# Kernel tuning notes

Hardware: AMD Instinct MI355X
Metric: run time of the kernel (lower is better)

The kernel has to match this reference:

```python
import jax, jax.numpy as jnp
import numpy as np

N = 50000        # nodes
E = 1600000      # edges (before self loops)
IN_DIM = 300     # input feature size
HID = 256        # hidden size
HEADS = 8
OC = HID // HEADS  # out channels per head = 32
LAYERS = 4
B = 1024         # number of target pairs
C = 3            # num classes
NEG_SLOPE = 0.2  # PyG GATConv leaky_relu slope


def setup_inputs() -> dict:
    key = jax.random.key(0)
    ks = jax.random.split(key, 12)

    def glorot(k, shape):
        lim = np.sqrt(6.0 / (shape[-2] + shape[-1]))
        return jax.random.uniform(k, shape, jnp.float32, -lim, lim)

    return {
        "x": jax.random.normal(ks[0], (N, IN_DIM), jnp.float32),
        "edge_index": jax.random.randint(ks[1], (2, E), 0, N, jnp.int64 if jax.config.jax_enable_x64 else jnp.int32),
        "target_mask": jax.random.randint(ks[2], (B, 2), 0, N, jnp.int64 if jax.config.jax_enable_x64 else jnp.int32),
        # lin1: [IN_DIM, HID] (stored pre-transposed vs torch)
        "lin1_W": glorot(ks[3], (IN_DIM, HID)),
        "lin1_b": jnp.zeros((HID,), jnp.float32),
        # stacked GATConv params
        "convs_W": glorot(ks[4], (LAYERS, HID, HEADS * OC)),
        "convs_att_dst": glorot(ks[5], (LAYERS, HEADS, OC)),  # att half applied to x_i (target)
        "convs_att_src": glorot(ks[6], (LAYERS, HEADS, OC)),  # att half applied to x_j (source)
        "convs_b": jnp.zeros((LAYERS, HID), jnp.float32),
        # lin3: [2*HID, C]
        "lin3_W": glorot(ks[7], (2 * HID, C)),
        "lin3_b": jnp.zeros((C,), jnp.float32),
    }


def gat_layer(h, src, tgt, W, att_dst, att_src, bias):
    """PyG-style GATConv (concat heads), edge list already includes self loops.
    h: [N, HID]; src/tgt: [E+N]; W: [HID, HEADS*OC]."""
    hw = (h @ W).reshape(N, HEADS, OC)
    # per-node attention scores, gathered per-edge (avoids materializing concat features)
    s_dst = jnp.einsum("nho,ho->nh", hw, att_dst)  # score for target role
    s_src = jnp.einsum("nho,ho->nh", hw, att_src)  # score for source role
    alpha = jax.nn.leaky_relu(s_dst[tgt] + s_src[src], NEG_SLOPE)  # [Etot, HEADS]
    # softmax over edges sharing the same target node (self loops => no empty segments)
    m = jax.ops.segment_max(alpha, tgt, num_segments=N)
    ex = jnp.exp(alpha - m[tgt])
    denom = jax.ops.segment_sum(ex, tgt, num_segments=N)
    a = ex / (denom[tgt] + 1e-16)
    # weighted scatter-aggregate of source features
    out = jax.ops.segment_sum(hw[src] * a[:, :, None], tgt, num_segments=N)  # [N, HEADS, OC]
    return out.reshape(N, HEADS * OC) + bias


def reference(x, edge_index, target_mask, lin1_W, lin1_b, convs_W,
              convs_att_dst, convs_att_src, convs_b, lin3_W, lin3_b):
    # add self loops once (PyG GATConv does this per layer; same edge set every layer)
    loop = jnp.arange(N, dtype=edge_index.dtype)
    src = jnp.concatenate([edge_index[0], loop])
    tgt = jnp.concatenate([edge_index[1], loop])

    h = x @ lin1_W + lin1_b
    for l in range(LAYERS):
        h = jax.nn.elu(gat_layer(h, src, tgt, convs_W[l],
                                 convs_att_dst[l], convs_att_src[l], convs_b[l]))
    # gather the two target nodes per sample and flatten -> [B, 2*HID]
    feats = h[target_mask].reshape(B, 2 * HID)
    logits = feats @ lin3_W + lin3_b
    return logits
```

## Files before the change

### kernel.cpp

```cpp
#include <hip/hip_runtime.h>
#include <math.h>

#define N_NODES 50000
#define N_PAD   50048
#define E_EDGES 1600000
#define ETOT    (E_EDGES + N_NODES)
#define EPAD    (E_EDGES + 8 * N_NODES)
#define IN_DIM  300
#define KP1     320
#define HID     256
#define HEADS   8
#define OC      32
#define LAYERS  4
#define BSAMP   1024
#define NEG_SLOPE 0.2f
#define NS1     (N_NODES + 1)

#define NB     8
#define NPB    6250
#define BCAP   262144
#define NBLK_P 512
#define NBLK_S 196
#define NBLK_B 2048
#define NAGG   2048

typedef unsigned long long ull;
typedef unsigned short u16;
typedef _Float16 half8 __attribute__((ext_vector_type(8)));
typedef _Float16 half4v __attribute__((ext_vector_type(4)));
typedef float f32x4 __attribute__((ext_vector_type(4)));

#define GLDS16(g, l) __builtin_amdgcn_global_load_lds( \
    (const __attribute__((address_space(1))) void*)(g), \
    (__attribute__((address_space(3))) void*)(l), 16, 0, 0)


__global__ __launch_bounds__(256) void part_count_kernel(const int* __restrict__ tgt,
                                                         int* __restrict__ gcount) {
    __shared__ int cnt[NB];
    if (threadIdx.x < NB) cnt[threadIdx.x] = 0;
    __syncthreads();
    const int chunk = (ETOT + NBLK_P - 1) / NBLK_P;
    int beg = blockIdx.x * chunk;
    int end = min(beg + chunk, ETOT);
    for (int e = beg + threadIdx.x; e < end; e += 256) {
        int t_ = (e < E_EDGES) ? tgt[e] : (e - E_EDGES);
        atomicAdd(&cnt[t_ / NPB], 1);
    }
    __syncthreads();
    if (threadIdx.x < NB) gcount[blockIdx.x * NB + threadIdx.x] = cnt[threadIdx.x];
}

__global__ __launch_bounds__(512) void part_scan_kernel(const int* __restrict__ gcount,
                                                        int* __restrict__ goff,
                                                        int* __restrict__ bcnt) {
    __shared__ int arr[NBLK_P][NB];
    int k = threadIdx.x;
    int4 a = ((const int4*)gcount)[k * 2];
    int4 b = ((const int4*)gcount)[k * 2 + 1];
    int own[NB] = {a.x, a.y, a.z, a.w, b.x, b.y, b.z, b.w};
    #pragma unroll
    for (int j = 0; j < NB; j++) arr[k][j] = own[j];
    __syncthreads();
    for (int off = 1; off < NBLK_P; off <<= 1) {
        int tmp[NB];
        #pragma unroll
        for (int j = 0; j < NB; j++) tmp[j] = (k >= off) ? arr[k - off][j] : 0;
        __syncthreads();
        #pragma unroll
        for (int j = 0; j < NB; j++) arr[k][j] += tmp[j];
        __syncthreads();
    }
    int ex[NB];
    #pragma unroll
    for (int j = 0; j < NB; j++) ex[j] = arr[k][j] - own[j];
    ((int4*)goff)[k * 2]     = make_int4(ex[0], ex[1], ex[2], ex[3]);
    ((int4*)goff)[k * 2 + 1] = make_int4(ex[4], ex[5], ex[6], ex[7]);
    if (k == NBLK_P - 1) {
        #pragma unroll
        for (int j = 0; j < NB; j++) bcnt[j] = arr[k][j];
    }
}

__global__ __launch_bounds__(256) void part_scatter_kernel(const int* __restrict__ src,
                                                           const int* __restrict__ tgt,
                                                           const int* __restrict__ goff,
                                                           ull* __restrict__ bpart) {
    __shared__ int cur[NB];
    if (threadIdx.x < NB) cur[threadIdx.x] = goff[blockIdx.x * NB + threadIdx.x];
    __syncthreads();
    const int chunk = (ETOT + NBLK_P - 1) / NBLK_P;
    int beg = blockIdx.x * chunk;
    int end = min(beg + chunk, ETOT);
    for (int e = beg + threadIdx.x; e < end; e += 256) {
        int s_, t_;
        if (e < E_EDGES) { s_ = src[e]; t_ = tgt[e]; }
        else             { s_ = t_ = e - E_EDGES; }
        int b = t_ / NPB;
        int pos = atomicAdd(&cur[b], 1);
        bpart[(size_t)b * BCAP + pos] = ((ull)(unsigned)t_ << 32) | (unsigned)s_;
    }
}

__global__ __launch_bounds__(256) void count_edges_kernel(const ull* __restrict__ bpart,
                                                          const int* __restrict__ bcnt,
                                                          int* counts) {
    int b = blockIdx.x & (NB - 1);
    int ib = blockIdx.x >> 3;
    int nblk = gridDim.x >> 3;
    int nb = bcnt[b];
    const ull* bp = bpart + (size_t)b * BCAP;
    for (int i = ib * 256 + threadIdx.x; i < nb; i += nblk * 256)
        atomicAdd(&counts[(int)(bp[i] >> 32)], 1);
}

__global__ __launch_bounds__(256) void scan1_kernel(const int* __restrict__ counts,
                                                    int* __restrict__ row_ptr,
                                                    int* __restrict__ bsum) {
    __shared__ int sums[256];
    int t = threadIdx.x;
    int i = blockIdx.x * 256 + t;
    int c = (i < N_NODES) ? ((counts[i] + 7) & ~7) : 0;
    sums[t] = c;
    __syncthreads();
    for (int off = 1; off < 256; off <<= 1) {
        int a = sums[t];
        int u = (t >= off) ? sums[t - off] : 0;
        __syncthreads();
        sums[t] = a + u;
        __syncthreads();
    }
    if (i < N_NODES) row_ptr[i] = sums[t] - c;
    if (t == 255) bsum[blockIdx.x] = sums[255];
}

__global__ __launch_bounds__(256) void scan2_kernel(const int* __restrict__ bsum,
                                                    int* __restrict__ boff,
                                                    int* __restrict__ row_ptr) {
    __shared__ int sums[256];
    int t = threadIdx.x;
    int b = (t < NBLK_S) ? bsum[t] : 0;
    sums[t] = b;
    __syncthreads();
    for (int off = 1; off < 256; off <<= 1) {
        int a = sums[t];
        int u = (t >= off) ? sums[t - off] : 0;
        __syncthreads();
        sums[t] = a + u;
        __syncthreads();
    }
    if (t < NBLK_S) boff[t] = sums[t] - b;
    if (t == 255) row_ptr[N_NODES] = sums[255];
}

__global__ __launch_bounds__(256) void scan3_kernel(int* __restrict__ row_ptr,
                                                    const int* __restrict__ boff,
                                                    int* __restrict__ cursor) {
    int i = blockIdx.x * 256 + threadIdx.x;
    if (i >= N_NODES) return;
    int v = row_ptr[i] + boff[blockIdx.x];
    row_ptr[i] = v;
    cursor[i]  = v;
}

__global__ __launch_bounds__(256) void fill_edges_kernel(const ull* __restrict__ bpart,
                                                         const int* __restrict__ bcnt,
                                                         int* cursor, u16* __restrict__ col) {
    int b = blockIdx.x & (NB - 1);
    int ib = blockIdx.x >> 3;
    int nblk = gridDim.x >> 3;
    int nb = bcnt[b];
    const ull* bp = bpart + (size_t)b * BCAP;
    for (int i = ib * 256 + threadIdx.x; i < nb; i += nblk * 256) {
        ull pk = bp[i];
        int t_ = (int)(pk >> 32);
        int s_ = (int)pk;
        int pos = atomicAdd(&cursor[t_], 1);
        col[pos] = (u16)s_;
    }
}

__global__ __launch_bounds__(256) void pad_edges_kernel(const int* __restrict__ cursor,
                                                        const int* __restrict__ row_ptr,
                                                        u16* __restrict__ col) {
    int i = blockIdx.x * 256 + threadIdx.x;
    if (i >= N_NODES) return;
    int e = cursor[i];
    int pe = row_ptr[i + 1];
    for (; e < pe; e++) col[e] = (u16)N_NODES;
}


__global__ __launch_bounds__(256) void cast_x_kernel(const float* __restrict__ x, _Float16* __restrict__ xh) {
    int i = blockIdx.x * 256 + threadIdx.x;
    if (i >= N_NODES * (KP1 / 8)) return;
    int r = i / (KP1 / 8), c8 = i % (KP1 / 8);
    half8 o;
    const float4* xr = (const float4*)(x + (size_t)r * IN_DIM);
    if (c8 < 37) {
        float4 u = xr[c8 * 2], v = xr[c8 * 2 + 1];
        o[0] = (_Float16)u.x; o[1] = (_Float16)u.y; o[2] = (_Float16)u.z; o[3] = (_Float16)u.w;
        o[4] = (_Float16)v.x; o[5] = (_Float16)v.y; o[6] = (_Float16)v.z; o[7] = (_Float16)v.w;
    } else if (c8 == 37) {
        float4 u = xr[74];
        o[0] = (_Float16)u.x; o[1] = (_Float16)u.y; o[2] = (_Float16)u.z; o[3] = (_Float16)u.w;
        o[4] = o[5] = o[6] = o[7] = (_Float16)0.f;
    } else {
        #pragma unroll
        for (int j = 0; j < 8; j++) o[j] = (_Float16)0.f;
    }
    ((half8*)xh)[i] = o;
}

__global__ __launch_bounds__(256) void cast_w1_kernel(const float* __restrict__ W, _Float16* __restrict__ Wt) {
    int i = blockIdx.x * 256 + threadIdx.x;
    if (i >= HID * KP1) return;
    int n = i / KP1, k = i % KP1;
    float v = (k < IN_DIM) ? W[(size_t)k * HID + n] : 0.f;
    Wt[i] = (_Float16)v;
}

__global__ __launch_bounds__(256) void cast_wc_kernel(const float* __restrict__ W, _Float16* __restrict__ Wt) {
    int i = blockIdx.x * 256 + threadIdx.x;
    if (i >= LAYERS * HID * HID) return;
    int l = i / (HID * HID);
    int r = i % (HID * HID);
    int n = r / HID, k = r % HID;
    Wt[i] = (_Float16)W[(size_t)l * HID * HID + (size_t)k * HID + n];
}

__global__ __launch_bounds__(256) void gemm_mfma_kernel(const _Float16* __restrict__ A,
                                                        const _Float16* __restrict__ Wt,
                                                        const float* __restrict__ bias,
                                                        _Float16* __restrict__ C,
                                                        int M, int Kp, int addbias,
                                                        int headmajor) {
    __shared__ _Float16 As[128][32];
    __shared__ _Float16 Bs[128][32];
    const int tid = threadIdx.x;
    const int m0 = blockIdx.x * 128;
    const int n0 = blockIdx.y * 128;
    const int w = tid >> 6, lane = tid & 63;
    const int wm = (w & 1) * 64, wn = (w >> 1) * 64;
    const int quad = lane >> 4, m16 = lane & 15;

    f32x4 acc[4][4];
    #pragma unroll
    for (int i = 0; i < 4; i++)
        #pragma unroll
        for (int j = 0; j < 4; j++)
            acc[i][j] = (f32x4){0.f, 0.f, 0.f, 0.f};

    char* lA = (char*)&As[0][0] + w * 1024;
    char* lB = (char*)&Bs[0][0] + w * 1024;

    for (int k0 = 0; k0 < Kp; k0 += 32) {
        #pragma unroll
        for (int i = 0; i < 2; i++) {
            int seg = tid + i * 256;
            int row = seg >> 2, off = seg & 3;
            GLDS16(&A[(size_t)(m0 + row) * Kp + k0 + off * 8], lA + i * 4096);
            GLDS16(&Wt[(size_t)(n0 + row) * Kp + k0 + off * 8], lB + i * 4096);
        }
        __syncthreads();

        half8 af[4], bf[4];
        #pragma unroll
        for (int i = 0; i < 4; i++) {
            af[i] = *(const half8*)&As[wm + i * 16 + m16][quad * 8];
            bf[i] = *(const half8*)&Bs[wn + i * 16 + m16][quad * 8];
        }
        #pragma unroll
        for (int mi = 0; mi < 4; mi++)
            #pragma unroll
            for (int ni = 0; ni < 4; ni++)
                acc[mi][ni] = __builtin_amdgcn_mfma_f32_16x16x32_f16(af[mi], bf[ni], acc[mi][ni], 0, 0, 0);
        __syncthreads();
    }

    #pragma unroll
    for (int mi = 0; mi < 4; mi++) {
        #pragma unroll
        for (int r = 0; r < 4; r++) {
            int row = m0 + wm + mi * 16 + quad * 4 + r;
            if (row < M) {
                #pragma unroll
                for (int ni = 0; ni < 4; ni++) {
                    int colg = n0 + wn + ni * 16 + m16;
                    float v = acc[mi][ni][r];
                    if (addbias) v += bias[colg];
                    if (headmajor) {
                        int hd = colg >> 5, oc = colg & 31;
                        C[((size_t)hd * N_NODES + row) * 32 + oc] = (_Float16)v;
                    } else {
                        C[(size_t)row * HID + colg] = (_Float16)v;
                    }
                }
            }
        }
    }
}

__global__ __launch_bounds__(256) void score_kernel(const _Float16* __restrict__ hw,
                                                    const float* __restrict__ att_dst,
                                                    const float* __restrict__ att_src,
                                                    float* __restrict__ s_dst,
                                                    float* __restrict__ s_src) {
    if (blockIdx.x == 0 && threadIdx.x < HEADS)
        s_src[(size_t)threadIdx.x * NS1 + N_NODES] = -1e30f;
    int wv = threadIdx.x >> 6, lane = threadIdx.x & 63;
    int nd = lane >> 3, hd = lane & 7;
    float4 ad[8], as4[8];
    const float4* A4d = (const float4*)att_dst;
    const float4* A4s = (const float4*)att_src;
    #pragma unroll
    for (int j = 0; j < 8; j++) { ad[j] = A4d[hd * 8 + j]; as4[j] = A4s[hd * 8 + j]; }
    const half8* hw8 = (const half8*)hw;
    int nwaves = gridDim.x * 4;
    for (int g = blockIdx.x * 4 + wv; g < N_NODES / 8; g += nwaves) {
        int node = g * 8 + nd;
        float sd = 0.f, ss = 0.f;
        #pragma unroll
        for (int k = 0; k < 4; k++) {
            half8 v = hw8[((size_t)hd * N_NODES + node) * 4 + k];
            #pragma unroll
            for (int i = 0; i < 8; i++) {
                float f = (float)v[i];
                int q = k * 8 + i;
                sd += f * ((const float*)&ad[q >> 2])[q & 3];
                ss += f * ((const float*)&as4[q >> 2])[q & 3];
            }
        }
        s_dst[(size_t)hd * N_NODES + node] = sd;
        s_src[(size_t)hd * NS1 + node] = ss;
    }
}

__global__ __launch_bounds__(256, 8) void agg_kernel(const int* __restrict__ row_ptr,
                                                     const u16* __restrict__ col,
                                                     const float* __restrict__ s_dst,
                                                     const float* __restrict__ s_src,
                                                     const _Float16* __restrict__ hw,
                                                     const float* __restrict__ bias,
                                                     _Float16* __restrict__ h_out) {
    __shared__ float exL[4][2][128];
    __shared__ int   snL[4][2][128];

    const int wv   = threadIdx.x >> 6;
    const int lane = threadIdx.x & 63;
    const int head = blockIdx.x & (NB - 1);
    const int ib   = blockIdx.x >> 3;
    const int nh   = lane >> 5;
    const int es   = (lane >> 2) & 7;
    const int cl   = lane & 3;
    const int wid  = ib * 4 + wv;
    const int NW   = (NAGG / NB) * 4;

    const float* sdh = s_dst + (size_t)head * N_NODES;
    const float* ssh = s_src + (size_t)head * NS1;
    const char*  hwh = (const char*)(hw + (size_t)head * N_NODES * 32);
    const unsigned vcl = (unsigned)(cl * 16);

    float bb[8];
    {
        const float* bpt = bias + head * 32 + cl * 8;
        #pragma unroll
        for (int i = 0; i < 8; i++) bb[i] = bpt[i];
    }

    float* exw = &exL[wv][nh][0];
    int*   snw = &snL[wv][nh][0];

    auto stage = [&](int s, int startg, int csz, float sdv) {
        float* exd = &exL[wv][s][0];
        int*   snd = &snL[wv][s][0];
        for (int b = 0; b < csz; b += 64) {
            int slot = b + lane;
            if (slot < csz) {
                int sn = (int)col[startg + slot];
                float a = sdv + ssh[(unsigned)sn];
                a = fmaxf(a, NEG_SLOPE * a);
                exd[slot] = __expf(a);
                snd[slot] = sn << 6;
            }
        }
    };

    float dsum, a0, a1, a2, a3, a4, a5, a6, a7;

    auto phaseC = [&](int ngrp) {
        int d0 = snw[es];
        int d1 = (ngrp > 1) ? snw[8 + es] : 0;
        half8 v0 = *(const half8*)(hwh + ((unsigned)d0 | vcl));
        for (int g = 0; g < ngrp; g++) {
            int d2 = (g + 2 < ngrp) ? snw[(g + 2) * 8 + es] : 0;
            half8 vn = *(const half8*)(hwh + ((unsigned)d1 | vcl));
            float e = exw[g * 8 + es];
            dsum += e;
            a0 += e * (float)v0[0];
            a1 += e * (float)v0[1];
            a2 += e * (float)v0[2];
            a3 += e * (float)v0[3];
            a4 += e * (float)v0[4];
            a5 += e * (float)v0[5];
            a6 += e * (float)v0[6];
            a7 += e * (float)v0[7];
            v0 = vn; d1 = d2;
        }
    };

    for (int tb = wid * 2; tb < N_NODES; tb += NW * 2) {
        int r0 = row_ptr[tb];
        int r1 = row_ptr[tb + 1];
        int r2 = row_ptr[tb + 2];
        int pd0 = r1 - r0, pd1 = r2 - r1;
        float sdv0 = sdh[tb], sdv1 = sdh[tb + 1];

        dsum = 0.f;
        a0 = a1 = a2 = a3 = a4 = a5 = a6 = a7 = 0.f;

        if (pd0 <= 128 && pd1 <= 128) {
            int mx = max(pd0, pd1);
            stage(0, r0, pd0, sdv0);
            stage(1, r1, pd1, sdv1);
            for (int slot = pd0 + lane; slot < mx; slot += 64) {
                exL[wv][0][slot] = 0.f; snL[wv][0][slot] = 0;
            }
            for (int slot = pd1 + lane; slot < mx; slot += 64) {
                exL[wv][1][slot] = 0.f; snL[wv][1][slot] = 0;
            }
            phaseC(mx >> 3);
        } else {
            #pragma unroll 1
            for (int s = 0; s < 2; s++) {
                for (int slot = lane; slot < 128; slot += 64) {
                    exL[wv][s ^ 1][slot] = 0.f; snL[wv][s ^ 1][slot] = 0;
                }
                int rs = s ? r1 : r0;
                int pds = s ? pd1 : pd0;
                float sdvs = s ? sdv1 : sdv0;
                for (int c0 = 0; c0 < pds; c0 += 128) {
                    int csz = min(pds - c0, 128);
                    stage(s, rs + c0, csz, sdvs);
                    phaseC(csz >> 3);
                }
            }
        }

        #pragma unroll
        for (int off = 4; off <= 16; off <<= 1) {
            dsum += __shfl_xor(dsum, off);
            a0 += __shfl_xor(a0, off);
            a1 += __shfl_xor(a1, off);
            a2 += __shfl_xor(a2, off);
            a3 += __shfl_xor(a3, off);
            a4 += __shfl_xor(a4, off);
            a5 += __shfl_xor(a5, off);
            a6 += __shfl_xor(a6, off);
            a7 += __shfl_xor(a7, off);
        }

        if (es == 0) {
            float inv = 1.f / (dsum + 1e-16f);
            float o[8] = {a0 * inv + bb[0], a1 * inv + bb[1],
                          a2 * inv + bb[2], a3 * inv + bb[3],
                          a4 * inv + bb[4], a5 * inv + bb[5],
                          a6 * inv + bb[6], a7 * inv + bb[7]};
            half8 ov;
            #pragma unroll
            for (int i = 0; i < 8; i++) {
                float v = (o[i] > 0.f) ? o[i] : (__expf(o[i]) - 1.f);
                ov[i] = (_Float16)v;
            }
            *(half8*)(h_out + (size_t)(tb + nh) * HID + head * 32 + cl * 8) = ov;
        }
    }
}

__global__ __launch_bounds__(256) void head_kernel(const _Float16* __restrict__ h,
                                                   const int* __restrict__ target_mask,
                                                   const float* __restrict__ W,
                                                   const float* __restrict__ b,
                                                   float* __restrict__ out) {
    int s = blockIdx.x;
    int t = threadIdx.x;
    int n0 = target_mask[s * 2 + 0];
    int n1 = target_mask[s * 2 + 1];
    float f0 = (float)h[(size_t)n0 * HID + t];
    float f1 = (float)h[(size_t)n1 * HID + t];
    float a0 = f0 * W[t * 3 + 0] + f1 * W[(t + 256) * 3 + 0];
    float a1 = f0 * W[t * 3 + 1] + f1 * W[(t + 256) * 3 + 1];
    float a2 = f0 * W[t * 3 + 2] + f1 * W[(t + 256) * 3 + 2];
    #pragma unroll
    for (int off = 32; off >= 1; off >>= 1) {
        a0 += __shfl_xor(a0, off);
        a1 += __shfl_xor(a1, off);
        a2 += __shfl_xor(a2, off);
    }
    __shared__ float red[4][3];
    int wv = t >> 6, ln = t & 63;
    if (ln == 0) { red[wv][0] = a0; red[wv][1] = a1; red[wv][2] = a2; }
    __syncthreads();
    if (t < 3) {
        out[s * 3 + t] = red[0][t] + red[1][t] + red[2][t] + red[3][t] + b[t];
    }
}


extern "C" void kernel_launch(void* const* d_in, const int* in_sizes, int n_in,
                              void* d_out, int out_size, void* d_ws, size_t ws_size,
                              hipStream_t stream) {
    const float* x        = (const float*)d_in[0];
    const int*   eidx     = (const int*)  d_in[1];
    const int*   tmask    = (const int*)  d_in[2];
    const float* lin1_W   = (const float*)d_in[3];
    const float* lin1_b   = (const float*)d_in[4];
    const float* convs_W  = (const float*)d_in[5];
    const float* att_dst  = (const float*)d_in[6];
    const float* att_src  = (const float*)d_in[7];
    const float* convs_b  = (const float*)d_in[8];
    const float* lin3_W   = (const float*)d_in[9];
    const float* lin3_b   = (const float*)d_in[10];
    float* out = (float*)d_out;

    char* ws = (char*)d_ws;
    size_t off = 0;
    auto alloc = [&](size_t bytes) -> void* {
        void* p = ws + off;
        off = (off + bytes + 255) & ~(size_t)255;
        return p;
    };
    _Float16* xh   = (_Float16*)alloc((size_t)N_PAD * KP1 * 2);
    _Float16* h    = (_Float16*)alloc((size_t)N_PAD * HID * 2);
    _Float16* hw   = (_Float16*)alloc((size_t)N_PAD * HID * 2);
    _Float16* w1t  = (_Float16*)alloc((size_t)HID * KP1 * 2);
    _Float16* wct  = (_Float16*)alloc((size_t)LAYERS * HID * HID * 2);
    float* sdst    = (float*)alloc((size_t)HEADS * N_NODES * 4);
    float* ssrc    = (float*)alloc((size_t)HEADS * NS1 * 4);
    int*   counts  = (int*)  alloc((size_t)N_NODES * 4);
    int*   rowptr  = (int*)  alloc((size_t)(N_NODES + 1) * 4);
    int*   cursor  = (int*)  alloc((size_t)N_NODES * 4);
    u16*   col     = (u16*)  alloc((size_t)(EPAD + 32) * 2);
    ull*   bpart   = (ull*)  alloc((size_t)NB * BCAP * 8);
    int*   bcnt    = (int*)  alloc((size_t)NB * 4);
    int*   gcount  = (int*)  alloc((size_t)NBLK_P * NB * 4);
    int*   goff    = (int*)  alloc((size_t)NBLK_P * NB * 4);
    int*   bsum    = (int*)  alloc((size_t)NBLK_S * 4);
    int*   boff    = (int*)  alloc((size_t)NBLK_S * 4);

    const int* src = eidx;
    const int* tgt = eidx + E_EDGES;

    hipMemsetAsync(counts, 0, (size_t)N_NODES * 4, stream);
    part_count_kernel<<<NBLK_P, 256, 0, stream>>>(tgt, gcount);
    part_scan_kernel<<<1, NBLK_P, 0, stream>>>(gcount, goff, bcnt);
    part_scatter_kernel<<<NBLK_P, 256, 0, stream>>>(src, tgt, goff, bpart);
    count_edges_kernel<<<NBLK_B, 256, 0, stream>>>(bpart, bcnt, counts);
    scan1_kernel<<<NBLK_S, 256, 0, stream>>>(counts, rowptr, bsum);
    scan2_kernel<<<1, 256, 0, stream>>>(bsum, boff, rowptr);
    scan3_kernel<<<NBLK_S, 256, 0, stream>>>(rowptr, boff, cursor);
    fill_edges_kernel<<<NBLK_B, 256, 0, stream>>>(bpart, bcnt, cursor, col);
    pad_edges_kernel<<<(N_NODES + 255) / 256, 256, 0, stream>>>(cursor, rowptr, col);

    cast_x_kernel<<<(N_NODES * (KP1 / 8) + 255) / 256, 256, 0, stream>>>(x, xh);
    cast_w1_kernel<<<(HID * KP1 + 255) / 256, 256, 0, stream>>>(lin1_W, w1t);
    cast_wc_kernel<<<(LAYERS * HID * HID + 255) / 256, 256, 0, stream>>>(convs_W, wct);

    gemm_mfma_kernel<<<dim3((N_NODES + 127) / 128, HID / 128), 256, 0, stream>>>(
        xh, w1t, lin1_b, h, N_NODES, KP1, 1, 0);

    for (int l = 0; l < LAYERS; l++) {
        gemm_mfma_kernel<<<dim3((N_NODES + 127) / 128, HID / 128), 256, 0, stream>>>(
            h, wct + (size_t)l * HID * HID, nullptr, hw, N_NODES, HID, 0, 1);
        score_kernel<<<512, 256, 0, stream>>>(
            hw, att_dst + (size_t)l * HEADS * OC, att_src + (size_t)l * HEADS * OC, sdst, ssrc);
        agg_kernel<<<NAGG, 256, 0, stream>>>(
            rowptr, col, sdst, ssrc, hw, convs_b + (size_t)l * HID, h);
    }

    head_kernel<<<BSAMP, 256, 0, stream>>>(h, tmask, lin3_W, lin3_b, out);
}
```

Before: 988.9 us.

## Software-pipeline GAT aggregation: prefetch next node pair's edges into double-buffered LDS

```diff
diff --git a/kernel.cpp b/kernel.cpp
--- a/kernel.cpp
+++ b/kernel.cpp
@@ -22,12 +22,12 @@
 #define NBLK_P 512
 #define NBLK_S 196
 #define NBLK_B 2048
-#define NAGG   2048
+#define NAGG   1536
+#define NW2    ((NAGG / NB) * 4 * 2)
 
 typedef unsigned long long ull;
 typedef unsigned short u16;
 typedef _Float16 half8 __attribute__((ext_vector_type(8)));
-typedef _Float16 half4v __attribute__((ext_vector_type(4)));
 typedef float f32x4 __attribute__((ext_vector_type(4)));
 
 #define GLDS16(g, l) __builtin_amdgcn_global_load_lds( \
@@ -336,15 +336,14 @@
     }
 }
 
-__global__ __launch_bounds__(256, 8) void agg_kernel(const int* __restrict__ row_ptr,
+__global__ __launch_bounds__(256, 6) void agg_kernel(const int* __restrict__ row_ptr,
                                                      const u16* __restrict__ col,
                                                      const float* __restrict__ s_dst,
                                                      const float* __restrict__ s_src,
                                                      const _Float16* __restrict__ hw,
                                                      const float* __restrict__ bias,
                                                      _Float16* __restrict__ h_out) {
-    __shared__ float exL[4][2][128];
-    __shared__ int   snL[4][2][128];
+    __shared__ ull pkL[4][2][2][128];
 
     const int wv   = threadIdx.x >> 6;
     const int lane = threadIdx.x & 63;
@@ -354,48 +353,31 @@
     const int es   = (lane >> 2) & 7;
     const int cl   = lane & 3;
     const int wid  = ib * 4 + wv;
-    const int NW   = (NAGG / NB) * 4;
 
     const float* sdh = s_dst + (size_t)head * N_NODES;
     const float* ssh = s_src + (size_t)head * NS1;
     const char*  hwh = (const char*)(hw + (size_t)head * N_NODES * 32);
     const unsigned vcl = (unsigned)(cl * 16);
 
-    float bb[8];
-    {
-        const float* bpt = bias + head * 32 + cl * 8;
-        #pragma unroll
-        for (int i = 0; i < 8; i++) bb[i] = bpt[i];
-    }
-
-    float* exw = &exL[wv][nh][0];
-    int*   snw = &snL[wv][nh][0];
-
-    auto stage = [&](int s, int startg, int csz, float sdv) {
-        float* exd = &exL[wv][s][0];
-        int*   snd = &snL[wv][s][0];
-        for (int b = 0; b < csz; b += 64) {
-            int slot = b + lane;
-            if (slot < csz) {
-                int sn = (int)col[startg + slot];
-                float a = sdv + ssh[(unsigned)sn];
-                a = fmaxf(a, NEG_SLOPE * a);
-                exd[slot] = __expf(a);
-                snd[slot] = sn << 6;
-            }
+    float dsum, a0, a1, a2, a3, a4, a5, a6, a7;
+
+    auto wr = [&](ull* pkd, int slot, int mx_, float sdv, float ss, int sn) {
+        if (slot < mx_) {
+            float a = sdv + ss;
+            a = fmaxf(a, NEG_SLOPE * a);
+            float ex = __expf(a);
+            pkd[slot] = ((ull)__float_as_uint(ex) << 32) | (unsigned)(sn << 6);
         }
     };
 
-    float dsum, a0, a1, a2, a3, a4, a5, a6, a7;
-
-    auto phaseC = [&](int ngrp) {
-        int d0 = snw[es];
-        int d1 = (ngrp > 1) ? snw[8 + es] : 0;
-        half8 v0 = *(const half8*)(hwh + ((unsigned)d0 | vcl));
+    auto phaseC = [&](const ull* pkw, int ngrp) {
+        ull p0 = pkw[es];
+        ull p1 = (ngrp > 1) ? pkw[8 + es] : 0;
+        half8 v0 = *(const half8*)(hwh + ((unsigned)(p0 & 0xffffffffu) | vcl));
         for (int g = 0; g < ngrp; g++) {
-            int d2 = (g + 2 < ngrp) ? snw[(g + 2) * 8 + es] : 0;
-            half8 vn = *(const half8*)(hwh + ((unsigned)d1 | vcl));
-            float e = exw[g * 8 + es];
+            ull p2 = (g + 2 < ngrp) ? pkw[(g + 2) * 8 + es] : 0;
+            half8 vn = *(const half8*)(hwh + ((unsigned)(p1 & 0xffffffffu) | vcl));
+            float e = __uint_as_float((unsigned)(p0 >> 32));
             dsum += e;
             a0 += e * (float)v0[0];
             a1 += e * (float)v0[1];
@@ -405,48 +387,11 @@
             a5 += e * (float)v0[5];
             a6 += e * (float)v0[6];
             a7 += e * (float)v0[7];
-            v0 = vn; d1 = d2;
+            p0 = p1; p1 = p2; v0 = vn;
         }
     };
 
-    for (int tb = wid * 2; tb < N_NODES; tb += NW * 2) {
-        int r0 = row_ptr[tb];
-        int r1 = row_ptr[tb + 1];
-        int r2 = row_ptr[tb + 2];
-        int pd0 = r1 - r0, pd1 = r2 - r1;
-        float sdv0 = sdh[tb], sdv1 = sdh[tb + 1];
-
-        dsum = 0.f;
-        a0 = a1 = a2 = a3 = a4 = a5 = a6 = a7 = 0.f;
-
-        if (pd0 <= 128 && pd1 <= 128) {
-            int mx = max(pd0, pd1);
-            stage(0, r0, pd0, sdv0);
-            stage(1, r1, pd1, sdv1);
-            for (int slot = pd0 + lane; slot < mx; slot += 64) {
-                exL[wv][0][slot] = 0.f; snL[wv][0][slot] = 0;
-            }
-            for (int slot = pd1 + lane; slot < mx; slot += 64) {
-                exL[wv][1][slot] = 0.f; snL[wv][1][slot] = 0;
-            }
-            phaseC(mx >> 3);
-        } else {
-            #pragma unroll 1
-            for (int s = 0; s < 2; s++) {
-                for (int slot = lane; slot < 128; slot += 64) {
-                    exL[wv][s ^ 1][slot] = 0.f; snL[wv][s ^ 1][slot] = 0;
-                }
-                int rs = s ? r1 : r0;
-                int pds = s ? pd1 : pd0;
-                float sdvs = s ? sdv1 : sdv0;
-                for (int c0 = 0; c0 < pds; c0 += 128) {
-                    int csz = min(pds - c0, 128);
-                    stage(s, rs + c0, csz, sdvs);
-                    phaseC(csz >> 3);
-                }
-            }
-        }
-
+    auto finish = [&](int tbp) {
         #pragma unroll
         for (int off = 4; off <= 16; off <<= 1) {
             dsum += __shfl_xor(dsum, off);
@@ -459,22 +404,124 @@
             a6 += __shfl_xor(a6, off);
             a7 += __shfl_xor(a7, off);
         }
-
         if (es == 0) {
+            const float* bpt = bias + head * 32 + cl * 8;
             float inv = 1.f / (dsum + 1e-16f);
-            float o[8] = {a0 * inv + bb[0], a1 * inv + bb[1],
-                          a2 * inv + bb[2], a3 * inv + bb[3],
-                          a4 * inv + bb[4], a5 * inv + bb[5],
-                          a6 * inv + bb[6], a7 * inv + bb[7]};
+            float o[8] = {a0 * inv + bpt[0], a1 * inv + bpt[1],
+                          a2 * inv + bpt[2], a3 * inv + bpt[3],
+                          a4 * inv + bpt[4], a5 * inv + bpt[5],
+                          a6 * inv + bpt[6], a7 * inv + bpt[7]};
             half8 ov;
             #pragma unroll
             for (int i = 0; i < 8; i++) {
                 float v = (o[i] > 0.f) ? o[i] : (__expf(o[i]) - 1.f);
                 ov[i] = (_Float16)v;
             }
-            *(half8*)(h_out + (size_t)(tb + nh) * HID + head * 32 + cl * 8) = ov;
-        }
-    }
+            *(half8*)(h_out + (size_t)(tbp + nh) * HID + head * 32 + cl * 8) = ov;
+        }
+    };
+
+    int cbig, cmx, cr0, cr1, cpd0, cpd1;
+    float csd0, csd1;
+    int tb = wid * 2;
+
+    {
+        cr0 = row_ptr[tb]; cr1 = row_ptr[tb + 1];
+        int r2 = row_ptr[tb + 2];
+        cpd0 = cr1 - cr0; cpd1 = r2 - cr1;
+        csd0 = sdh[tb]; csd1 = sdh[tb + 1];
+        cbig = (cpd0 > 128) || (cpd1 > 128);
+        cmx = max(cpd0, cpd1);
+        if (!cbig) {
+            int sA = N_NODES, sB = N_NODES, sC = N_NODES, sD = N_NODES;
+            if (lane < cpd0)      sA = (int)col[cr0 + lane];
+            if (lane + 64 < cpd0) sB = (int)col[cr0 + lane + 64];
+            if (lane < cpd1)      sC = (int)col[cr1 + lane];
+            if (lane + 64 < cpd1) sD = (int)col[cr1 + lane + 64];
+            float eA = ssh[(unsigned)sA], eB = ssh[(unsigned)sB];
+            float eC = ssh[(unsigned)sC], eD = ssh[(unsigned)sD];
+            wr(&pkL[wv][0][0][0], lane,      cmx, csd0, eA, sA);
+            wr(&pkL[wv][0][0][0], lane + 64, cmx, csd0, eB, sB);
+            wr(&pkL[wv][0][1][0], lane,      cmx, csd1, eC, sC);
+            wr(&pkL[wv][0][1][0], lane + 64, cmx, csd1, eD, sD);
+        }
+    }
+
+#define AGG_PROC(CUR, NXT)                                                     \
+    do {                                                                       \
+        int tn = tb + NW2;                                                     \
+        bool hn = tn < N_NODES;                                                \
+        int nbig = 0, nmx = 0, nr0 = 0, nr1 = 0, npd0 = 0, npd1 = 0;           \
+        float nsd0 = 0.f, nsd1 = 0.f;                                          \
+        int sA = N_NODES, sB = N_NODES, sC = N_NODES, sD = N_NODES;            \
+        if (hn) {                                                              \
+            nr0 = row_ptr[tn]; nr1 = row_ptr[tn + 1];                          \
+            int r2n = row_ptr[tn + 2];                                         \
+            npd0 = nr1 - nr0; npd1 = r2n - nr1;                                \
+            nsd0 = sdh[tn]; nsd1 = sdh[tn + 1];                                \
+            nbig = (npd0 > 128) || (npd1 > 128);                               \
+            nmx = max(npd0, npd1);                                             \
+            if (!nbig) {                                                       \
+                if (lane < npd0)      sA = (int)col[nr0 + lane];               \
+                if (lane + 64 < npd0) sB = (int)col[nr0 + lane + 64];          \
+                if (lane < npd1)      sC = (int)col[nr1 + lane];               \
+                if (lane + 64 < npd1) sD = (int)col[nr1 + lane + 64];          \
+            }                                                                  \
+        }                                                                      \
+        float eA = ssh[(unsigned)sA], eB = ssh[(unsigned)sB];                  \
+        float eC = ssh[(unsigned)sC], eD = ssh[(unsigned)sD];                  \
+        dsum = 0.f;                                                            \
+        a0 = a1 = a2 = a3 = a4 = a5 = a6 = a7 = 0.f;                           \
+        if (!cbig) {                                                           \
+            phaseC(&pkL[wv][CUR][nh][0], cmx >> 3);                            \
+        } else {                                                               \
+            for (int slot = lane; slot < 128; slot += 64) {                    \
+                pkL[wv][CUR][0][slot] = 0ull;                                  \
+                pkL[wv][CUR][1][slot] = 0ull;                                  \
+            }                                                                  \
+            for (int s = 0; s < 2; s++) {                                      \
+                int rs = s ? cr1 : cr0;                                        \
+                int pds = s ? cpd1 : cpd0;                                     \
+                float sdvs = s ? csd1 : csd0;                                  \
+                for (int c0 = 0; c0 < pds; c0 += 128) {                        \
+                    int csz = min(pds - c0, 128);                              \
+                    for (int b = 0; b < csz; b += 64) {                        \
+                        int slot = b + lane;                                   \
+                        if (slot < csz) {                                      \
+                            int sn = (int)col[rs + c0 + slot];                 \
+                            float a = sdvs + ssh[(unsigned)sn];                \
+                            a = fmaxf(a, NEG_SLOPE * a);                       \
+                            pkL[wv][CUR][s][slot] =                            \
+                                ((ull)__float_as_uint(__expf(a)) << 32) |      \
+                                (unsigned)(sn << 6);                           \
+                        }                                                      \
+                    }                                                          \
+                    phaseC(&pkL[wv][CUR][nh][0], csz >> 3);                    \
+                }                                                              \
+                for (int slot = lane; slot < 128; slot += 64)                  \
+                    pkL[wv][CUR][s][slot] = 0ull;                              \
+            }                                                                  \
+        }                                                                      \
+        if (hn && !nbig) {                                                     \
+            wr(&pkL[wv][NXT][0][0], lane,      nmx, nsd0, eA, sA);             \
+            wr(&pkL[wv][NXT][0][0], lane + 64, nmx, nsd0, eB, sB);             \
+            wr(&pkL[wv][NXT][1][0], lane,      nmx, nsd1, eC, sC);             \
+            wr(&pkL[wv][NXT][1][0], lane + 64, nmx, nsd1, eD, sD);             \
+        }                                                                      \
+        finish(tb);                                                            \
+        cbig = nbig; cmx = nmx; cr0 = nr0; cr1 = nr1;                          \
+        cpd0 = npd0; cpd1 = npd1; csd0 = nsd0; csd1 = nsd1;                    \
+    } while (0)
+
+    for (;;) {
+        AGG_PROC(0, 1);
+        tb += NW2;
+        if (tb >= N_NODES) break;
+        AGG_PROC(1, 0);
+        tb += NW2;
+        if (tb >= N_NODES) break;
+    }
+#undef AGG_PROC
 }
 
 __global__ __launch_bounds__(256) void head_kernel(const _Float16* __restrict__ h,
```

Result: slower. 1.078 ms (+9.0%).
